# Kernel tuning notes

Measured on AMD Instinct MI355X. Metric: run time of the kernel, lower is better.

## Reference

```python
import jax, jax.numpy as jnp
import numpy as np

D_MODEL = 1024
H = 16
D_K = D_MODEL // H


def setup_inputs() -> dict:
    key = jax.random.key(0)
    ks = jax.random.split(key, 7)
    B, S = 4, 2048
    scale = 1.0 / np.sqrt(D_MODEL)
    return {
        "q": jax.random.normal(ks[0], (B, S, D_MODEL), dtype=jnp.float32),
        "k": jax.random.normal(ks[1], (B, S, D_MODEL), dtype=jnp.float32),
        "v": jax.random.normal(ks[2], (B, S, D_MODEL), dtype=jnp.float32),
        "W_q": jax.random.normal(ks[3], (D_MODEL, D_MODEL), dtype=jnp.float32) * scale,
        "W_k": jax.random.normal(ks[4], (D_MODEL, D_MODEL), dtype=jnp.float32) * scale,
        "W_v": jax.random.normal(ks[5], (D_MODEL, D_MODEL), dtype=jnp.float32) * scale,
        "W_o": jax.random.normal(ks[6], (D_MODEL, D_MODEL), dtype=jnp.float32) * scale,
    }


def reference(q, k, v, W_q, W_k, W_v, W_o):
    B, S, _ = q.shape
    # nn.Linear(bias=False): y = x @ W.T
    def proj(x, W):
        return (x @ W.T).reshape(B, -1, H, D_K).transpose(0, 2, 1, 3)  # [B,H,S,d_k]
    Q = proj(q, W_q)
    K = proj(k, W_k)
    V = proj(v, W_v)
    scores = jnp.einsum('bhqd,bhkd->bhqk', Q, K) / jnp.sqrt(jnp.float32(D_K))
    attn = jax.nn.softmax(scores, axis=-1)  # dropout p=0.0 -> identity
    ctx = jnp.einsum('bhqk,bhkd->bhqd', attn, V)
    ctx = ctx.transpose(0, 2, 1, 3).reshape(B, S, H * D_K)
    return ctx @ W_o.T
```

## Files before the change

kernel.cpp:

```cpp
#include <hip/hip_runtime.h>
#include <stdint.h>


typedef __attribute__((ext_vector_type(8))) short bf16x8;
typedef __attribute__((ext_vector_type(4))) float f32x4;

__device__ __forceinline__ void lds_async16(const void* g, void* l) {
  __builtin_amdgcn_global_load_lds(
      (const __attribute__((address_space(1))) void*)g,
      (__attribute__((address_space(3))) void*)l, 16, 0, 0);
}

__device__ __forceinline__ unsigned short f2bf(float f) {
  union { float f; unsigned u; } v; v.f = f;
  unsigned u = v.u + 0x7fffu + ((v.u >> 16) & 1u);
  return (unsigned short)(u >> 16);
}

__device__ __forceinline__ float fast_exp2(float x) {
#if __has_builtin(__builtin_amdgcn_exp2f)
  return __builtin_amdgcn_exp2f(x);
#else
  return exp2f(x);
#endif
}

__device__ __forceinline__ unsigned pk2(float a, float b) {
#if __has_builtin(__builtin_amdgcn_cvt_pk_bf16_f32)
  typedef __bf16 bf16v2 __attribute__((ext_vector_type(2)));
  union { bf16v2 v; unsigned u; } x;
  x.v = __builtin_amdgcn_cvt_pk_bf16_f32(a, b);
  return x.u;
#else
  return (unsigned)f2bf(a) | ((unsigned)f2bf(b) << 16);
#endif
}

__global__ void cvt_kernel(const float* s0, const float* s1, const float* s2, const float* s3,
                           unsigned short* d0, unsigned short* d1, unsigned short* d2, unsigned short* d3,
                           int n4) {
  int which = blockIdx.y;
  const float* s = which == 0 ? s0 : which == 1 ? s1 : which == 2 ? s2 : s3;
  unsigned short* d = which == 0 ? d0 : which == 1 ? d1 : which == 2 ? d2 : d3;
  int i = blockIdx.x * 256 + threadIdx.x;
  if (i < n4) {
    float4 v = ((const float4*)s)[i];
    ushort4 o;
    o.x = f2bf(v.x); o.y = f2bf(v.y); o.z = f2bf(v.z); o.w = f2bf(v.w);
    ((ushort4*)d)[i] = o;
  }
}

struct GemmAcc { f32x4 acc[4][4]; };

__device__ __forceinline__ void gemm_core(const unsigned short* __restrict__ Arows,
                                          const unsigned short* __restrict__ Brows,
                                          int tm, int tn, unsigned short* As,
                                          unsigned short* Bs, GemmAcc& g) {
  constexpr int K = 1024;
  const int tid = threadIdx.x;
  const int lane = tid & 63;
  const int wv = tid >> 6;
  const int wm = wv & 1, wn = wv >> 1;
  const int c16 = lane & 15, q4 = lane >> 4;

#pragma unroll
  for (int i = 0; i < 4; ++i)
#pragma unroll
    for (int j = 0; j < 4; ++j)
#pragma unroll
      for (int r = 0; r < 4; ++r) g.acc[i][j][r] = 0.f;

  const int srow = tid >> 3;
  const int gc = (((tid & 7) ^ (srow & 7)) << 3);
  const unsigned short* Arow = Arows + (size_t)(tm * 128 + srow) * K + gc;
  const unsigned short* Brow = Brows + (size_t)(tn * 128 + srow) * K + gc;
  char* AsBase = (char*)As + tid * 16;
  char* BsBase = (char*)Bs + tid * 16;

  for (int k0 = 0; k0 < K; k0 += 64) {
    __syncthreads();
#pragma unroll
    for (int i = 0; i < 4; ++i) {
      lds_async16(Arow + k0 + i * 32 * K, AsBase + i * 4096);
      lds_async16(Brow + k0 + i * 32 * K, BsBase + i * 4096);
    }
    __syncthreads();
#pragma unroll
    for (int ks = 0; ks < 2; ++ks) {
      bf16x8 af[4], bfr[4];
#pragma unroll
      for (int i = 0; i < 4; ++i) {
        int mr = wm * 64 + i * 16 + c16;
        int pa = (ks * 4 + q4) ^ (mr & 7);
        af[i] = *(const bf16x8*)(As + mr * 64 + pa * 8);
        int nr = wn * 64 + i * 16 + c16;
        int pb = (ks * 4 + q4) ^ (nr & 7);
        bfr[i] = *(const bf16x8*)(Bs + nr * 64 + pb * 8);
      }
#pragma unroll
      for (int i = 0; i < 4; ++i)
#pragma unroll
        for (int j = 0; j < 4; ++j)
          g.acc[i][j] = __builtin_amdgcn_mfma_f32_16x16x32_bf16(af[i], bfr[j], g.acc[i][j], 0, 0, 0);
    }
  }
}

__global__ __launch_bounds__(256, 2)
void qkv_kernel(const unsigned short* __restrict__ qb, const unsigned short* __restrict__ kb,
                const unsigned short* __restrict__ vb,
                const unsigned short* __restrict__ wq, const unsigned short* __restrict__ wk,
                const unsigned short* __restrict__ wv_,
                unsigned short* __restrict__ Qb, unsigned short* __restrict__ Kb,
                unsigned short* __restrict__ Vtb) {
  __shared__ unsigned short As[128 * 64];
  __shared__ unsigned short Bs[128 * 64];
  const int z = blockIdx.z;
  const unsigned short* A;
  const unsigned short* B;
  int tm, tn;
  if (z == 0)      { A = qb;  B = wq;  tm = blockIdx.y; tn = blockIdx.x; }
  else if (z == 1) { A = kb;  B = wk;  tm = blockIdx.y; tn = blockIdx.x; }
  else             { A = wv_; B = vb;  tm = blockIdx.x; tn = blockIdx.y; }

  GemmAcc g;
  gemm_core(A, B, tm, tn, As, Bs, g);

  const int lane = threadIdx.x & 63;
  const int wv = threadIdx.x >> 6;
  const int wm = wv & 1, wn = wv >> 1;
  const int c16 = lane & 15, q4 = lane >> 4;
  const float qscale = 0.125f * 1.44269504f;

#pragma unroll
  for (int i = 0; i < 4; ++i)
#pragma unroll
    for (int j = 0; j < 4; ++j)
#pragma unroll
      for (int r = 0; r < 4; ++r) {
        int m = tm * 128 + wm * 64 + i * 16 + q4 * 4 + r;
        int n = tn * 128 + wn * 64 + j * 16 + c16;
        float val = g.acc[i][j][r];
        if (z < 2) {
          if (z == 0) val *= qscale;
          int b = m >> 11, s_ = m & 2047, h = n >> 6, d = n & 63;
          unsigned short* dst = z == 0 ? Qb : Kb;
          dst[(((size_t)(b * 16 + h) * 2048 + s_) << 6) | d] = f2bf(val);
        } else {
          int h = m >> 6, d = m & 63, b = n >> 11, s_ = n & 2047;
          int sl = s_ & 127;
          int sp = (sl & ~31) | (((sl >> 2) & 3) << 3) | (((sl >> 4) & 1) << 2) | (sl & 3);
          s_ = (s_ & ~127) | sp;
          Vtb[((size_t)((b * 16 + h) * 64 + d) << 11) | s_] = f2bf(val);
        }
      }
}

__global__ __launch_bounds__(256, 2)
void out_gemm(const unsigned short* __restrict__ A, const unsigned short* __restrict__ B,
              float* __restrict__ C) {
  __shared__ unsigned short As[128 * 64];
  __shared__ unsigned short Bs[128 * 64];
  GemmAcc g;
  gemm_core(A, B, blockIdx.y, blockIdx.x, As, Bs, g);
  const int lane = threadIdx.x & 63;
  const int wv = threadIdx.x >> 6;
  const int wm = wv & 1, wn = wv >> 1;
  const int c16 = lane & 15, q4 = lane >> 4;
#pragma unroll
  for (int i = 0; i < 4; ++i)
#pragma unroll
    for (int j = 0; j < 4; ++j)
#pragma unroll
      for (int r = 0; r < 4; ++r) {
        int m = blockIdx.y * 128 + wm * 64 + i * 16 + q4 * 4 + r;
        int n = blockIdx.x * 128 + wn * 64 + j * 16 + c16;
        C[(size_t)m * 1024 + n] = g.acc[i][j][r];
      }
}

__global__ __launch_bounds__(128, 2)
void attn_kernel(const unsigned short* __restrict__ Q,
                 const unsigned short* __restrict__ K,
                 const unsigned short* __restrict__ Vt,
                 unsigned short* __restrict__ ctx) {
  __shared__ unsigned short Ks[2][64 * 64];
  __shared__ unsigned short Vs[2][64 * 64];

  const int tid = threadIdx.x, lane = tid & 63, w = tid >> 6;
  const int c16 = lane & 15, q4 = lane >> 4;
  const int wbase = w * 64;
  const unsigned wgid = blockIdx.x;
  const int bh = (int)((wgid & 7u) * 8 + ((wgid >> 3) & 7u));
  const int qt = (int)(wgid >> 6);
  const unsigned short* Qp = Q + ((size_t)bh * 2048 + qt * 128) * 64;
  const unsigned short* Kp = K + (size_t)bh * 2048 * 64;
  const unsigned short* Vp = Vt + (size_t)bh * 64 * 2048;

  const int srow = tid >> 3;
  const int gcol = (((tid & 7) ^ (srow & 7)) << 3);

  {
    const unsigned short* Qr = Qp + (size_t)srow * 64 + gcol;
    char* base = (char*)Ks + tid * 16;
#pragma unroll
    for (int c = 0; c < 8; ++c) lds_async16(Qr + c * 16 * 64, base + c * 2048);
  }
  __syncthreads();
  const unsigned short* Kflat = &Ks[0][0];
  bf16x8 qf[4][2];
#pragma unroll
  for (int nn = 0; nn < 4; ++nn)
#pragma unroll
    for (int ks = 0; ks < 2; ++ks) {
      int qr = wbase + nn * 16 + c16;
      int pos = (ks * 4 + q4) ^ (qr & 7);
      qf[nn][ks] = *(const bf16x8*)(Kflat + qr * 64 + pos * 8);
    }
  __syncthreads();

  bf16x8 onesf;
  {
    short v = (c16 == 0) ? (short)0x3F80 : (short)0;
#pragma unroll
    for (int j = 0; j < 8; ++j) onesf[j] = v;
  }

  f32x4 oacc[4][4];
  f32x4 lacc[4];
#pragma unroll
  for (int nn = 0; nn < 4; ++nn) {
#pragma unroll
    for (int r = 0; r < 4; ++r) lacc[nn][r] = 0.f;
#pragma unroll
    for (int dj = 0; dj < 4; ++dj)
#pragma unroll
      for (int r = 0; r < 4; ++r) oacc[nn][dj][r] = 0.f;
  }

  const unsigned short* Kr0 = Kp + (size_t)srow * 64 + gcol;
  const unsigned short* Vr0 = Vp + (size_t)srow * 2048 + gcol;

  {
    char* kb = (char*)Ks[0] + tid * 16;
    char* vb = (char*)Vs[0] + tid * 16;
#pragma unroll
    for (int c = 0; c < 4; ++c) {
      lds_async16(Kr0 + (size_t)c * 16 * 64, kb + c * 2048);
      lds_async16(Vr0 + (size_t)c * 16 * 2048, vb + c * 2048);
    }
  }

  int cur = 0;
  for (int kt = 0; kt < 32; ++kt) {
    __syncthreads();
    if (kt < 31) {
      char* kb = (char*)Ks[cur ^ 1] + tid * 16;
      char* vb = (char*)Vs[cur ^ 1] + tid * 16;
      const unsigned short* Krn = Kr0 + (size_t)(kt + 1) * 64 * 64;
      const unsigned short* Vrn = Vr0 + (size_t)(kt + 1) * 64;
#pragma unroll
      for (int c = 0; c < 4; ++c) {
        lds_async16(Krn + (size_t)c * 16 * 64, kb + c * 2048);
        lds_async16(Vrn + (size_t)c * 16 * 2048, vb + c * 2048);
      }
    }

    const unsigned short* KsC = Ks[cur];
    const unsigned short* VsC = Vs[cur];

#pragma unroll
    for (int ks2 = 0; ks2 < 2; ++ks2) {
      f32x4 s[2][4];
      __builtin_amdgcn_s_setprio(1);
#pragma unroll
      for (int ms = 0; ms < 2; ++ms) {
        const int row = (ks2 * 2 + ms) * 16 + c16;
        const bf16x8 kf0 = *(const bf16x8*)(KsC + row * 64 + ((0 + q4) ^ (row & 7)) * 8);
        const bf16x8 kf1 = *(const bf16x8*)(KsC + row * 64 + ((4 + q4) ^ (row & 7)) * 8);
#pragma unroll
        for (int nn = 0; nn < 4; ++nn) {
          f32x4 z = {0.f, 0.f, 0.f, 0.f};
          z = __builtin_amdgcn_mfma_f32_16x16x32_bf16(kf0, qf[nn][0], z, 0, 0, 0);
          z = __builtin_amdgcn_mfma_f32_16x16x32_bf16(kf1, qf[nn][1], z, 0, 0, 0);
          s[ms][nn] = z;
        }
      }
      __builtin_amdgcn_s_setprio(0);
      bf16x8 vf[4];
#pragma unroll
      for (int dj = 0; dj < 4; ++dj) {
        const int dr = dj * 16 + c16;
        vf[dj] = *(const bf16x8*)(VsC + dr * 64 + (((ks2 * 4 + q4) ^ (dr & 7))) * 8);
      }
      bf16x8 pfv[4];
#pragma unroll
      for (int nn = 0; nn < 4; ++nn) {
        union PU { unsigned u[4]; bf16x8 v; } pf;
        pf.u[0] = pk2(fast_exp2(s[0][nn][0]), fast_exp2(s[0][nn][1]));
        pf.u[1] = pk2(fast_exp2(s[0][nn][2]), fast_exp2(s[0][nn][3]));
        pf.u[2] = pk2(fast_exp2(s[1][nn][0]), fast_exp2(s[1][nn][1]));
        pf.u[3] = pk2(fast_exp2(s[1][nn][2]), fast_exp2(s[1][nn][3]));
        pfv[nn] = pf.v;
      }
      __builtin_amdgcn_s_setprio(1);
#pragma unroll
      for (int nn = 0; nn < 4; ++nn)
        lacc[nn] = __builtin_amdgcn_mfma_f32_16x16x32_bf16(pfv[nn], onesf, lacc[nn], 0, 0, 0);
#pragma unroll
      for (int dj = 0; dj < 4; ++dj)
#pragma unroll
        for (int nn = 0; nn < 4; ++nn)
          oacc[nn][dj] = __builtin_amdgcn_mfma_f32_16x16x32_bf16(pfv[nn], vf[dj], oacc[nn][dj], 0, 0, 0);
      __builtin_amdgcn_s_setprio(0);
    }
    cur ^= 1;
  }

  int b = bh >> 4, h = bh & 15;
#pragma unroll
  for (int nn = 0; nn < 4; ++nn)
#pragma unroll
    for (int r = 0; r < 4; ++r) {
      float l = __shfl(lacc[nn][r], lane & 48, 64);
      float inv = 1.f / l;
      int s_ = qt * 128 + wbase + nn * 16 + q4 * 4 + r;
#pragma unroll
      for (int dj = 0; dj < 4; ++dj) {
        int d = dj * 16 + c16;
        ctx[((size_t)(b * 2048 + s_)) * 1024 + h * 64 + d] = f2bf(oacc[nn][dj][r] * inv);
      }
    }
}

extern "C" void kernel_launch(void* const* d_in, const int* in_sizes, int n_in,
                              void* d_out, int out_size, void* d_ws, size_t ws_size,
                              hipStream_t stream) {
  const float* q  = (const float*)d_in[0];
  const float* k  = (const float*)d_in[1];
  const float* v  = (const float*)d_in[2];
  const float* Wq = (const float*)d_in[3];
  const float* Wk = (const float*)d_in[4];
  const float* Wv = (const float*)d_in[5];
  const float* Wo = (const float*)d_in[6];

  char* ws = (char*)d_ws;
  unsigned short* qb  = (unsigned short*)(ws);
  unsigned short* kb  = (unsigned short*)(ws + (16u << 20));
  unsigned short* vb  = (unsigned short*)(ws + (32u << 20));
  unsigned short* wqb = (unsigned short*)(ws + (48u << 20));
  unsigned short* wkb = (unsigned short*)(ws + (50u << 20));
  unsigned short* wvb = (unsigned short*)(ws + (52u << 20));
  unsigned short* wob = (unsigned short*)(ws + (54u << 20));
  unsigned short* Qb  = (unsigned short*)(ws + (56u << 20));
  unsigned short* Kb  = (unsigned short*)(ws + (72u << 20));
  unsigned short* Vtb = (unsigned short*)(ws + (88u << 20));
  unsigned short* ctxb = qb;

  cvt_kernel<<<dim3(1024, 4), 256, 0, stream>>>(Wq, Wk, Wv, Wo, wqb, wkb, wvb, wob, 262144);
  cvt_kernel<<<dim3(8192, 3), 256, 0, stream>>>(q, k, v, q, qb, kb, vb, qb, 2097152);

  qkv_kernel<<<dim3(8, 64, 3), 256, 0, stream>>>(qb, kb, vb, wqb, wkb, wvb, Qb, Kb, Vtb);

  attn_kernel<<<dim3(1024), 128, 0, stream>>>(Qb, Kb, Vtb, ctxb);

  out_gemm<<<dim3(8, 64), 256, 0, stream>>>(ctxb, wob, (float*)d_out);
}
```

Measured before the change: 329.1 us.

## Replace 128x128 GEMM core with 256x256 double-buffered pipelined 8-wave tile

Rewrites the shared GEMM core used by the QKV projection and output projection. Each block now computes a 256x256 tile with 8 waves, and the K-steps are double-buffered through async global-to-LDS loads. Barriers and vmcnt waits are interleaved so loads for later K-steps overlap the MFMA work, and setprio is raised around MFMA clusters. The goal is more reuse per loaded byte and hidden load latency. The cost is 128KB of LDS per block, which may block the requested 2 blocks per CU, and fewer blocks in the grid (384 and 128), which can leave CUs underused.

```diff
diff --git a/kernel.cpp b/kernel.cpp
--- a/kernel.cpp
+++ b/kernel.cpp
@@ -51,71 +51,137 @@
   }
 }
 
-struct GemmAcc { f32x4 acc[4][4]; };
-
-__device__ __forceinline__ void gemm_core(const unsigned short* __restrict__ Arows,
-                                          const unsigned short* __restrict__ Brows,
-                                          int tm, int tn, unsigned short* As,
-                                          unsigned short* Bs, GemmAcc& g) {
-  constexpr int K = 1024;
+struct G256 { f32x4 acc[8][4]; };
+
+__device__ __forceinline__ void stage_half256(const unsigned short* __restrict__ src,
+                                              int rowbase, int kt, int h,
+                                              unsigned short* lds, int tid) {
+  const int srow = tid >> 3;
+  const int g = tid & 7;
+  const int col = ((g ^ (srow & 7)) << 3);
+  const unsigned short* s0 = src + (size_t)(rowbase + h * 128 + srow) * 1024 + kt * 64 + col;
+  char* d0 = (char*)lds + h * 16384 + tid * 16;
+  lds_async16(s0, d0);
+  lds_async16(s0 + (size_t)64 * 1024, d0 + 8192);
+}
+
+__device__ __forceinline__ void read_af(const unsigned short* buf, int wm, int c16, int q4,
+                                        int ibase, bf16x8 (&af)[4][2]) {
+#pragma unroll
+  for (int ii = 0; ii < 4; ++ii)
+#pragma unroll
+    for (int ks = 0; ks < 2; ++ks) {
+      int row = wm * 128 + (ibase + ii) * 16 + c16;
+      af[ii][ks] = *(const bf16x8*)(buf + row * 64 + (((ks * 4 + q4) ^ (row & 7)) * 8));
+    }
+}
+
+__device__ __forceinline__ void read_bf(const unsigned short* buf, int wn, int c16, int q4,
+                                        int jbase, bf16x8 (&bf)[2][2]) {
+#pragma unroll
+  for (int jj = 0; jj < 2; ++jj)
+#pragma unroll
+    for (int ks = 0; ks < 2; ++ks) {
+      int row = wn * 64 + (jbase + jj) * 16 + c16;
+      bf[jj][ks] = *(const bf16x8*)(buf + row * 64 + (((ks * 4 + q4) ^ (row & 7)) * 8));
+    }
+}
+
+__device__ __forceinline__ void mfma_quad(G256& G, const bf16x8 (&af)[4][2],
+                                          const bf16x8 (&bf)[2][2], int i0, int j0) {
+  __builtin_amdgcn_s_setprio(1);
+#pragma unroll
+  for (int ii = 0; ii < 4; ++ii)
+#pragma unroll
+    for (int jj = 0; jj < 2; ++jj)
+#pragma unroll
+      for (int ks = 0; ks < 2; ++ks)
+        G.acc[i0 + ii][j0 + jj] = __builtin_amdgcn_mfma_f32_16x16x32_bf16(
+            af[ii][ks], bf[jj][ks], G.acc[i0 + ii][j0 + jj], 0, 0, 0);
+  __builtin_amdgcn_s_setprio(0);
+}
+
+__device__ __forceinline__ void gemm256_core(const unsigned short* __restrict__ A,
+                                             const unsigned short* __restrict__ B,
+                                             int tm, int tn,
+                                             unsigned short* As0, unsigned short* As1,
+                                             unsigned short* Bs0, unsigned short* Bs1,
+                                             G256& G) {
   const int tid = threadIdx.x;
   const int lane = tid & 63;
   const int wv = tid >> 6;
-  const int wm = wv & 1, wn = wv >> 1;
+  const int wm = wv >> 2, wn = wv & 3;
   const int c16 = lane & 15, q4 = lane >> 4;
-
-#pragma unroll
-  for (int i = 0; i < 4; ++i)
+  const int am = tm * 256, bn = tn * 256;
+
+#pragma unroll
+  for (int i = 0; i < 8; ++i)
 #pragma unroll
     for (int j = 0; j < 4; ++j)
 #pragma unroll
-      for (int r = 0; r < 4; ++r) g.acc[i][j][r] = 0.f;
-
-  const int srow = tid >> 3;
-  const int gc = (((tid & 7) ^ (srow & 7)) << 3);
-  const unsigned short* Arow = Arows + (size_t)(tm * 128 + srow) * K + gc;
-  const unsigned short* Brow = Brows + (size_t)(tn * 128 + srow) * K + gc;
-  char* AsBase = (char*)As + tid * 16;
-  char* BsBase = (char*)Bs + tid * 16;
-
-  for (int k0 = 0; k0 < K; k0 += 64) {
-    __syncthreads();
-#pragma unroll
-    for (int i = 0; i < 4; ++i) {
-      lds_async16(Arow + k0 + i * 32 * K, AsBase + i * 4096);
-      lds_async16(Brow + k0 + i * 32 * K, BsBase + i * 4096);
-    }
-    __syncthreads();
-#pragma unroll
-    for (int ks = 0; ks < 2; ++ks) {
-      bf16x8 af[4], bfr[4];
-#pragma unroll
-      for (int i = 0; i < 4; ++i) {
-        int mr = wm * 64 + i * 16 + c16;
-        int pa = (ks * 4 + q4) ^ (mr & 7);
-        af[i] = *(const bf16x8*)(As + mr * 64 + pa * 8);
-        int nr = wn * 64 + i * 16 + c16;
-        int pb = (ks * 4 + q4) ^ (nr & 7);
-        bfr[i] = *(const bf16x8*)(Bs + nr * 64 + pb * 8);
-      }
-#pragma unroll
-      for (int i = 0; i < 4; ++i)
-#pragma unroll
-        for (int j = 0; j < 4; ++j)
-          g.acc[i][j] = __builtin_amdgcn_mfma_f32_16x16x32_bf16(af[i], bfr[j], g.acc[i][j], 0, 0, 0);
-    }
-  }
-}
-
-__global__ __launch_bounds__(256, 2)
+      for (int r = 0; r < 4; ++r) G.acc[i][j][r] = 0.f;
+
+  stage_half256(B, bn, 0, 0, Bs0, tid);
+  stage_half256(A, am, 0, 0, As0, tid);
+  stage_half256(B, bn, 0, 1, Bs0, tid);
+  stage_half256(A, am, 0, 1, As0, tid);
+  stage_half256(B, bn, 1, 0, Bs1, tid);
+  stage_half256(A, am, 1, 0, As1, tid);
+
+  bf16x8 af[4][2], bfa[2][2], bfb[2][2];
+
+  for (int i = 0; i < 8; ++i) {
+    const int t1 = 2 * i + 1, t2 = 2 * i + 2, t3 = 2 * i + 3;
+    const bool more = (i < 7);
+    asm volatile("s_waitcnt vmcnt(4)" ::: "memory");
+    __builtin_amdgcn_s_barrier();
+    stage_half256(B, bn, t1, 1, Bs1, tid);
+    read_af(As0, wm, c16, q4, 0, af);
+    read_bf(Bs0, wn, c16, q4, 0, bfa);
+    mfma_quad(G, af, bfa, 0, 0);
+    __builtin_amdgcn_s_barrier();
+    stage_half256(A, am, t1, 1, As1, tid);
+    read_bf(Bs0, wn, c16, q4, 2, bfb);
+    mfma_quad(G, af, bfb, 0, 2);
+    __builtin_amdgcn_s_barrier();
+    if (more) stage_half256(B, bn, t2, 0, Bs0, tid);
+    read_af(As0, wm, c16, q4, 4, af);
+    mfma_quad(G, af, bfb, 4, 2);
+    __builtin_amdgcn_s_barrier();
+    if (more) stage_half256(A, am, t2, 0, As0, tid);
+    mfma_quad(G, af, bfa, 4, 0);
+    if (more) { asm volatile("s_waitcnt vmcnt(4)" ::: "memory"); }
+    else      { asm volatile("s_waitcnt vmcnt(0)" ::: "memory"); }
+    __builtin_amdgcn_s_barrier();
+    if (more) stage_half256(B, bn, t2, 1, Bs0, tid);
+    read_af(As1, wm, c16, q4, 0, af);
+    read_bf(Bs1, wn, c16, q4, 0, bfa);
+    mfma_quad(G, af, bfa, 0, 0);
+    __builtin_amdgcn_s_barrier();
+    if (more) stage_half256(A, am, t2, 1, As0, tid);
+    read_bf(Bs1, wn, c16, q4, 2, bfb);
+    mfma_quad(G, af, bfb, 0, 2);
+    __builtin_amdgcn_s_barrier();
+    if (more) stage_half256(B, bn, t3, 0, Bs1, tid);
+    read_af(As1, wm, c16, q4, 4, af);
+    mfma_quad(G, af, bfb, 4, 2);
+    __builtin_amdgcn_s_barrier();
+    if (more) stage_half256(A, am, t3, 0, As1, tid);
+    mfma_quad(G, af, bfa, 4, 0);
+  }
+}
+
+__global__ __launch_bounds__(512, 2)
 void qkv_kernel(const unsigned short* __restrict__ qb, const unsigned short* __restrict__ kb,
                 const unsigned short* __restrict__ vb,
                 const unsigned short* __restrict__ wq, const unsigned short* __restrict__ wk,
                 const unsigned short* __restrict__ wv_,
                 unsigned short* __restrict__ Qb, unsigned short* __restrict__ Kb,
                 unsigned short* __restrict__ Vtb) {
-  __shared__ unsigned short As[128 * 64];
-  __shared__ unsigned short Bs[128 * 64];
+  __shared__ unsigned short As0[256 * 64];
+  __shared__ unsigned short As1[256 * 64];
+  __shared__ unsigned short Bs0[256 * 64];
+  __shared__ unsigned short Bs1[256 * 64];
   const int z = blockIdx.z;
   const unsigned short* A;
   const unsigned short* B;
@@ -124,24 +190,24 @@
   else if (z == 1) { A = kb;  B = wk;  tm = blockIdx.y; tn = blockIdx.x; }
   else             { A = wv_; B = vb;  tm = blockIdx.x; tn = blockIdx.y; }
 
-  GemmAcc g;
-  gemm_core(A, B, tm, tn, As, Bs, g);
+  G256 G;
+  gemm256_core(A, B, tm, tn, As0, As1, Bs0, Bs1, G);
 
   const int lane = threadIdx.x & 63;
   const int wv = threadIdx.x >> 6;
-  const int wm = wv & 1, wn = wv >> 1;
+  const int wm = wv >> 2, wn = wv & 3;
   const int c16 = lane & 15, q4 = lane >> 4;
   const float qscale = 0.125f * 1.44269504f;
 
 #pragma unroll
-  for (int i = 0; i < 4; ++i)
+  for (int i = 0; i < 8; ++i)
 #pragma unroll
     for (int j = 0; j < 4; ++j)
 #pragma unroll
       for (int r = 0; r < 4; ++r) {
-        int m = tm * 128 + wm * 64 + i * 16 + q4 * 4 + r;
-        int n = tn * 128 + wn * 64 + j * 16 + c16;
-        float val = g.acc[i][j][r];
+        int m = tm * 256 + wm * 128 + i * 16 + q4 * 4 + r;
+        int n = tn * 256 + wn * 64 + j * 16 + c16;
+        float val = G.acc[i][j][r];
         if (z < 2) {
           if (z == 0) val *= qscale;
           int b = m >> 11, s_ = m & 2047, h = n >> 6, d = n & 63;
@@ -157,26 +223,28 @@
       }
 }
 
-__global__ __launch_bounds__(256, 2)
+__global__ __launch_bounds__(512, 2)
 void out_gemm(const unsigned short* __restrict__ A, const unsigned short* __restrict__ B,
               float* __restrict__ C) {
-  __shared__ unsigned short As[128 * 64];
-  __shared__ unsigned short Bs[128 * 64];
-  GemmAcc g;
-  gemm_core(A, B, blockIdx.y, blockIdx.x, As, Bs, g);
+  __shared__ unsigned short As0[256 * 64];
+  __shared__ unsigned short As1[256 * 64];
+  __shared__ unsigned short Bs0[256 * 64];
+  __shared__ unsigned short Bs1[256 * 64];
+  G256 G;
+  gemm256_core(A, B, blockIdx.y, blockIdx.x, As0, As1, Bs0, Bs1, G);
   const int lane = threadIdx.x & 63;
   const int wv = threadIdx.x >> 6;
-  const int wm = wv & 1, wn = wv >> 1;
+  const int wm = wv >> 2, wn = wv & 3;
   const int c16 = lane & 15, q4 = lane >> 4;
 #pragma unroll
-  for (int i = 0; i < 4; ++i)
+  for (int i = 0; i < 8; ++i)
 #pragma unroll
     for (int j = 0; j < 4; ++j)
 #pragma unroll
       for (int r = 0; r < 4; ++r) {
-        int m = blockIdx.y * 128 + wm * 64 + i * 16 + q4 * 4 + r;
-        int n = blockIdx.x * 128 + wn * 64 + j * 16 + c16;
-        C[(size_t)m * 1024 + n] = g.acc[i][j][r];
+        int m = blockIdx.y * 256 + wm * 128 + i * 16 + q4 * 4 + r;
+        int n = blockIdx.x * 256 + wn * 64 + j * 16 + c16;
+        C[(size_t)m * 1024 + n] = G.acc[i][j][r];
       }
 }
 
@@ -361,9 +429,9 @@
   cvt_kernel<<<dim3(1024, 4), 256, 0, stream>>>(Wq, Wk, Wv, Wo, wqb, wkb, wvb, wob, 262144);
   cvt_kernel<<<dim3(8192, 3), 256, 0, stream>>>(q, k, v, q, qb, kb, vb, qb, 2097152);
 
-  qkv_kernel<<<dim3(8, 64, 3), 256, 0, stream>>>(qb, kb, vb, wqb, wkb, wvb, Qb, Kb, Vtb);
+  qkv_kernel<<<dim3(4, 32, 3), 512, 0, stream>>>(qb, kb, vb, wqb, wkb, wvb, Qb, Kb, Vtb);
 
   attn_kernel<<<dim3(1024), 128, 0, stream>>>(Qb, Kb, Vtb, ctxb);
 
-  out_gemm<<<dim3(8, 64), 256, 0, stream>>>(ctxb, wob, (float*)d_out);
-}
+  out_gemm<<<dim3(4, 32), 512, 0, stream>>>(ctxb, wob, (float*)d_out);
+}
```

Measured after the change: 354.7 us. 7.8% more time.
